# Kernel tuning notes

Hardware: AMD Instinct MI355X
Metric: run time of the kernel (lower is better)

The kernel has to match this reference:

```python
import jax, jax.numpy as jnp
import numpy as np

B, N, K, E, H, A = 16384, 200000, 16, 256, 2, 64
HD = E // H  # head_dim = 128


def setup_inputs() -> dict:
    key = jax.random.key(0)
    ks = jax.random.split(key, 10)
    s = 0.02
    return {
        "center_idx": jax.random.randint(ks[0], (B,), 0, N),
        "emb_table": jax.random.normal(ks[1], (N, E), jnp.float32),
        "neighbor_idx": jax.random.randint(ks[2], (N, K), 0, N),
        "neighbor_wt": jax.random.uniform(ks[3], (N, K), dtype=jnp.float32),
        # per-head attention MLP: Linear(2E -> A), GELU, Linear(A -> 1); stacked over heads
        "attn_W1": jax.random.normal(ks[4], (H, 2 * E, A), jnp.float32) * s,
        "attn_b1": jnp.zeros((H, A), jnp.float32),
        "attn_W2": jax.random.normal(ks[5], (H, A), jnp.float32) * s,
        "attn_b2": jnp.zeros((H,), jnp.float32),
        # per-head gate: Linear(HD -> HD), torch convention y = x @ W.T + b
        "gate_W": jax.random.normal(ks[6], (H, HD, HD), jnp.float32) * s,
        "gate_b": jnp.zeros((H, HD), jnp.float32),
        "out_W": jax.random.normal(ks[7], (E, E), jnp.float32) * s,
        "out_b": jnp.zeros((E,), jnp.float32),
    }


def reference(center_idx, emb_table, neighbor_idx, neighbor_wt,
              attn_W1, attn_b1, attn_W2, attn_b2,
              gate_W, gate_b, out_W, out_b):
    valid = center_idx >= 0                                      # [B]
    safe = jnp.maximum(center_idx, 0)
    center = jnp.where(valid[:, None], emb_table[safe], 0.0)      # [B,E]

    nb_idx = neighbor_idx[safe]                                   # [B,K]
    nb_wt = neighbor_wt[safe]                                     # [B,K]
    nb_mask = nb_idx >= 0
    nb_emb = emb_table[jnp.maximum(nb_idx, 0)]                    # [B,K,E]

    pair = jnp.concatenate(
        [jnp.broadcast_to(center[:, None, :], nb_emb.shape), nb_emb], axis=-1)  # [B,K,2E]

    # both attention heads in one einsum (exact GELU, as torch nn.GELU default)
    h1 = jax.nn.gelu(jnp.einsum('bkf,hfa->bkha', pair, attn_W1) + attn_b1,
                     approximate=False)                           # [B,K,H,A]
    logits = jnp.einsum('bkha,ha->bhk', h1, attn_W2) + attn_b2[None, :, None]  # [B,H,K]
    logits = logits + jnp.log(nb_wt + 1e-8)[:, None, :]
    logits = jnp.where(nb_mask[:, None, :], logits, -jnp.inf)
    has_any = jnp.any(nb_mask, axis=-1)                           # [B]
    logits = jnpp_where = jnp.where(has_any[:, None, None], logits, 0.0)
    w = jax.nn.softmax(logits, axis=-1)                           # [B,H,K]; dropout is identity in eval

    # aggregated[:, h*HD:(h+1)*HD] for head h == head-block of head-h weighted sum
    nb_r = nb_emb.reshape(-1, K, H, HD)
    agg = jnp.einsum('bhk,bkhd->bhd', w, nb_r)                    # [B,H,HD]

    c_head = center.reshape(-1, H, HD)
    gate = jax.nn.sigmoid(jnp.einsum('bhd,hed->bhe', c_head, gate_W) + gate_b)
    combined = (c_head + gate * agg).reshape(-1, E)               # [B,E]

    out = combined @ out_W.T + out_b
    return jnp.where(valid[:, None], out, center)
```

## Files before the change

### kernel.cpp

```cpp
#include <hip/hip_runtime.h>
#include <hip/hip_bf16.h>
#include <math.h>

#define BATCH   16384
#define NTAB    200000
#define KNB     16
#define EDIM    256
#define HEADS   2
#define ADIM    64
#define HD      128

typedef __attribute__((ext_vector_type(8))) short  short8;
typedef __attribute__((ext_vector_type(4))) float  f32x4;
typedef __attribute__((ext_vector_type(8))) unsigned short ushort8;
typedef __attribute__((ext_vector_type(4))) unsigned short ushort4v;

__device__ __forceinline__ unsigned short f2b(float f) {
    union { float f; unsigned u; } x; x.f = f;
    unsigned r = x.u + 0x7fffu + ((x.u >> 16) & 1u);
    return (unsigned short)(r >> 16);
}
__device__ __forceinline__ float b2f(unsigned short h) {
    union { unsigned u; float f; } x; x.u = ((unsigned)h) << 16;
    return x.f;
}

static const size_t OFF_TBL  = 0;
static const size_t OFF_T    = OFF_TBL  + (size_t)NTAB * 256 * 2;
static const size_t OFF_CG   = OFF_T    + (size_t)NTAB * 128 * 2;
static const size_t OFF_COMB = OFF_CG   + (size_t)BATCH * 384 * 2;
static const size_t OFF_WCAT = OFF_COMB + (size_t)BATCH * 256 * 2;
static const size_t OFF_W1B  = OFF_WCAT + 384 * 256 * 2;
static const size_t OFF_OUTW = OFF_W1B  + 128 * 256 * 2;
static const size_t OFF_BCAT = OFF_OUTW + 256 * 256 * 2;

__global__ __launch_bounds__(256) void repack_kernel(
    const float* __restrict__ W1, const float* __restrict__ gateW,
    const float* __restrict__ outW,
    const float* __restrict__ b1, const float* __restrict__ gateB,
    unsigned short* __restrict__ WcatT, unsigned short* __restrict__ W1bT,
    unsigned short* __restrict__ outWT, float* __restrict__ bcat)
{
    int i = blockIdx.x * 256 + threadIdx.x;
    {
        int c = i >> 8, f = i & 255;
        float v;
        if (c < 128) {
            int h = c >> 6, a = c & 63;
            v = W1[h * 32768 + f * 64 + a];
        } else {
            int e = c - 128;
            int h = e >> 7;
            v = ((e >> 7) == (f >> 7)) ? gateW[h * 16384 + (e & 127) * 128 + (f & 127)] : 0.f;
        }
        WcatT[i] = f2b(v);
    }
    if (i < 32768) {
        int c = i >> 8, f = i & 255;
        int h = c >> 6, a = c & 63;
        W1bT[i] = f2b(W1[h * 32768 + (256 + f) * 64 + a]);
    }
    if (i < 65536) outWT[i] = f2b(outW[i]);
    if (i < 384) bcat[i] = (i < 128) ? b1[i] : gateB[i - 128];
}

template<int AMODE, bool OUT_BF16, bool HAS_BIAS, bool HAS_MASK, bool WRITE_ABF>
__global__ __launch_bounds__(256) void gemm_mfma(
    const float* __restrict__ Af, const unsigned short* __restrict__ Ab,
    unsigned short* __restrict__ AoutBf,
    const int* __restrict__ gather,
    const unsigned short* __restrict__ Wt, int Nw,
    const float* __restrict__ bias, const int* __restrict__ mask,
    void* __restrict__ Cout, int M)
{
    __shared__ unsigned short sA[128 * 32];
    __shared__ unsigned short sB[128 * 32];
    __shared__ int s_idx[128];

    const int t = threadIdx.x;
    const int row0    = blockIdx.x * 128;
    const int colBase = blockIdx.y * 128;

    if (AMODE == 1 && t < 128) s_idx[t] = gather[row0 + t];

    const int wv   = t >> 6;
    const int wr   = wv >> 1, wc = wv & 1;
    const int lane = t & 63;
    const int l15  = lane & 15;
    const int quad = lane >> 4;

    f32x4 acc[4][4];
#pragma unroll
    for (int a = 0; a < 4; ++a)
#pragma unroll
        for (int b = 0; b < 4; ++b) acc[a][b] = (f32x4)0.f;

    for (int k0 = 0; k0 < 256; k0 += 32) {
        __syncthreads();
        if (AMODE == 0) {
#pragma unroll
            for (int l = 0; l < 4; ++l) {
                int p = t + l * 256;
                int row = p >> 3, seg = p & 7;
                int gr = row0 + row;
                int sr = gr < M ? gr : M - 1;
                const float4 v = *(const float4*)&Af[(size_t)sr * 256 + k0 + seg * 4];
                ushort4v h;
                h.x = f2b(v.x); h.y = f2b(v.y); h.z = f2b(v.z); h.w = f2b(v.w);
                *(ushort4v*)&sA[row * 32 + seg * 4] = h;
                if (WRITE_ABF && gr < M)
                    *(ushort4v*)&AoutBf[(size_t)gr * 256 + k0 + seg * 4] = h;
            }
        } else {
#pragma unroll
            for (int l = 0; l < 2; ++l) {
                int p = t + l * 256;
                int row = p >> 2, seg = p & 3;
                int sr;
                if (AMODE == 1) { int g = s_idx[row]; sr = g < 0 ? 0 : g; }
                else            { sr = row0 + row; if (sr > M - 1) sr = M - 1; }
                const unsigned short* gsrc = Ab + (size_t)sr * 256 + k0 + seg * 8;
                unsigned short* lbase = sA + (size_t)(p & ~63) * 8;
                __builtin_amdgcn_global_load_lds(
                    (const __attribute__((address_space(1))) void*)gsrc,
                    (__attribute__((address_space(3))) void*)lbase, 16, 0, 0);
            }
        }
#pragma unroll
        for (int l = 0; l < 2; ++l) {
            int p = t + l * 256;
            int n = p >> 2, seg = p & 3;
            const unsigned short* gsrc = Wt + (size_t)(colBase + n) * 256 + k0 + seg * 8;
            unsigned short* lbase = sB + (size_t)(p & ~63) * 8;
            __builtin_amdgcn_global_load_lds(
                (const __attribute__((address_space(1))) void*)gsrc,
                (__attribute__((address_space(3))) void*)lbase, 16, 0, 0);
        }
        __syncthreads();

        short8 af[4], bfr[4];
#pragma unroll
        for (int tr = 0; tr < 4; ++tr)
            af[tr] = *(const short8*)&sA[(wr * 64 + tr * 16 + l15) * 32 + quad * 8];
#pragma unroll
        for (int tc = 0; tc < 4; ++tc)
            bfr[tc] = *(const short8*)&sB[(wc * 64 + tc * 16 + l15) * 32 + quad * 8];
#pragma unroll
        for (int tr = 0; tr < 4; ++tr)
#pragma unroll
            for (int tc = 0; tc < 4; ++tc)
                acc[tr][tc] = __builtin_amdgcn_mfma_f32_16x16x32_bf16(
                    af[tr], bfr[tc], acc[tr][tc], 0, 0, 0);
    }

    float bcol[4];
#pragma unroll
    for (int tc = 0; tc < 4; ++tc)
        bcol[tc] = HAS_BIAS ? bias[colBase + wc * 64 + tc * 16 + l15] : 0.f;

#pragma unroll
    for (int tr = 0; tr < 4; ++tr) {
#pragma unroll
        for (int r = 0; r < 4; ++r) {
            int rowg = row0 + wr * 64 + tr * 16 + quad * 4 + r;
            if (rowg < M) {
                bool zero = HAS_MASK && (mask[rowg] < 0);
#pragma unroll
                for (int tc = 0; tc < 4; ++tc) {
                    int col = colBase + wc * 64 + tc * 16 + l15;
                    float v = zero ? 0.f : acc[tr][tc][r] + bcol[tc];
                    if (OUT_BF16)
                        ((unsigned short*)Cout)[(size_t)rowg * Nw + col] = f2b(v);
                    else
                        ((float*)Cout)[(size_t)rowg * Nw + col] = v;
                }
            }
        }
    }
}

__global__ __launch_bounds__(256) void epilogue_kernel(
    const unsigned short* __restrict__ tableBf, const int* __restrict__ center_idx,
    const int* __restrict__ nb_idx_tab, const float* __restrict__ nb_wt_tab,
    const unsigned short* __restrict__ T, const unsigned short* __restrict__ cg,
    const float* __restrict__ W2, const float* __restrict__ b2,
    unsigned short* __restrict__ comb)
{
    const int b = blockIdx.x;
    const int t = threadIdx.x;

    __shared__ float s_cg[384];
    __shared__ float s_w2[128];
    __shared__ float s_logit[32];
    __shared__ float s_wmx[32];
    __shared__ int   s_nb[16];
    __shared__ float s_wt[16];

    const int ci   = center_idx[b];
    const int safe = ci < 0 ? 0 : ci;

    if (t < 16) {
        s_nb[t] = nb_idx_tab[(size_t)safe * KNB + t];
        s_wt[t] = nb_wt_tab[(size_t)safe * KNB + t];
    }
    if (t < 128) s_w2[t] = W2[t];
    for (int i = t; i < 384; i += 256) s_cg[i] = b2f(cg[(size_t)b * 384 + i]);
    const float ctr = (ci < 0) ? 0.f : b2f(tableBf[(size_t)ci * 256 + t]);
    __syncthreads();

    {
        const int k = t >> 4, s = t & 15;
        const int nb = s_nb[k];
        const int ns = nb < 0 ? 0 : nb;
        const ushort8 tv = *(const ushort8*)&T[(size_t)ns * 128 + s * 8];
        float partial = 0.f;
#pragma unroll
        for (int j = 0; j < 8; ++j) {
            int c = s * 8 + j;
            float v = b2f(tv[j]) + s_cg[c];
            float g = 0.5f * v * (1.f + erff(v * 0.70710678118654752440f));
            partial = fmaf(g, s_w2[c], partial);
        }
        partial += __shfl_xor(partial, 1, 64);
        partial += __shfl_xor(partial, 2, 64);
        partial += __shfl_xor(partial, 4, 64);
        if (s == 0) s_logit[k] = partial;
        if (s == 8) s_logit[16 + k] = partial;
    }
    __syncthreads();

    if (t < 32) {
        const int h = t >> 4, k = t & 15;
        const int nb = s_nb[k];
        unsigned long long bm = __ballot(nb >= 0);
        const bool hasany = ((bm >> (h * 16)) & 0xFFFFull) != 0ull;
        float L = (nb >= 0)
            ? s_logit[h * 16 + k] + b2[h] + logf(s_wt[k] + 1e-8f)
            : -INFINITY;
        float m = L;
        m = fmaxf(m, __shfl_xor(m, 1, 16));
        m = fmaxf(m, __shfl_xor(m, 2, 16));
        m = fmaxf(m, __shfl_xor(m, 4, 16));
        m = fmaxf(m, __shfl_xor(m, 8, 16));
        float e = (nb >= 0) ? expf(L - m) : 0.f;
        float ssum = e;
        ssum += __shfl_xor(ssum, 1, 16);
        ssum += __shfl_xor(ssum, 2, 16);
        ssum += __shfl_xor(ssum, 4, 16);
        ssum += __shfl_xor(ssum, 8, 16);
        s_wmx[t] = hasany ? e / ssum : (1.f / 16.f);
    }
    __syncthreads();

    const int h = t >> 7;
    float agg = 0.f;
#pragma unroll
    for (int k = 0; k < 16; ++k) {
        int nb = s_nb[k];
        int ns = nb < 0 ? 0 : nb;
        agg = fmaf(s_wmx[h * 16 + k], b2f(tableBf[(size_t)ns * 256 + t]), agg);
    }
    float gl   = s_cg[128 + t];
    float gate = 1.f / (1.f + expf(-gl));
    comb[(size_t)b * 256 + t] = f2b(ctr + gate * agg);
}

extern "C" void kernel_launch(void* const* d_in, const int* in_sizes, int n_in,
                              void* d_out, int out_size, void* d_ws, size_t ws_size,
                              hipStream_t stream)
{
    const int*   center_idx = (const int*)  d_in[0];
    const float* emb_table  = (const float*)d_in[1];
    const int*   nb_idx     = (const int*)  d_in[2];
    const float* nb_wt      = (const float*)d_in[3];
    const float* attn_W1    = (const float*)d_in[4];
    const float* attn_b1    = (const float*)d_in[5];
    const float* attn_W2    = (const float*)d_in[6];
    const float* attn_b2    = (const float*)d_in[7];
    const float* gate_W     = (const float*)d_in[8];
    const float* gate_b     = (const float*)d_in[9];
    const float* out_W      = (const float*)d_in[10];
    const float* out_b      = (const float*)d_in[11];
    float* out = (float*)d_out;

    char* ws = (char*)d_ws;
    unsigned short* tableBf = (unsigned short*)(ws + OFF_TBL);
    unsigned short* T       = (unsigned short*)(ws + OFF_T);
    unsigned short* cgB     = (unsigned short*)(ws + OFF_CG);
    unsigned short* comb    = (unsigned short*)(ws + OFF_COMB);
    unsigned short* WcatT   = (unsigned short*)(ws + OFF_WCAT);
    unsigned short* W1bT    = (unsigned short*)(ws + OFF_W1B);
    unsigned short* outWT   = (unsigned short*)(ws + OFF_OUTW);
    float*          bcat    = (float*)         (ws + OFF_BCAT);

    repack_kernel<<<384, 256, 0, stream>>>(attn_W1, gate_W, out_W, attn_b1, gate_b,
                                           WcatT, W1bT, outWT, bcat);

    gemm_mfma<0, true, false, false, true><<<dim3((NTAB + 127) / 128, 1), 256, 0, stream>>>(
        emb_table, nullptr, tableBf, nullptr, W1bT, 128, nullptr, nullptr, T, NTAB);

    gemm_mfma<1, true, true, false, false><<<dim3(BATCH / 128, 3), 256, 0, stream>>>(
        nullptr, tableBf, nullptr, center_idx, WcatT, 384, bcat, nullptr, cgB, BATCH);

    epilogue_kernel<<<BATCH, 256, 0, stream>>>(
        tableBf, center_idx, nb_idx, nb_wt, T, cgB, attn_W2, attn_b2, comb);

    gemm_mfma<2, false, true, true, false><<<dim3(BATCH / 128, 2), 256, 0, stream>>>(
        nullptr, comb, nullptr, nullptr, outWT, 256, out_b, center_idx, out, BATCH);
}
```

Baseline: 461.8 us.

## Replace table-wide GEMM with register-resident weight streaming kernel

Measured after the change: 468.5 us. About the same (+1.4%).

```diff
diff --git a/kernel.cpp b/kernel.cpp
--- a/kernel.cpp
+++ b/kernel.cpp
@@ -64,10 +64,62 @@
     if (i < 384) bcat[i] = (i < 128) ? b1[i] : gateB[i - 128];
 }
 
-template<int AMODE, bool OUT_BF16, bool HAS_BIAS, bool HAS_MASK, bool WRITE_ABF>
+__global__ __launch_bounds__(256) void tgemm_stream(
+    const float* __restrict__ Af, const unsigned short* __restrict__ Wt,
+    unsigned short* __restrict__ T, unsigned short* __restrict__ tableBf)
+{
+    const int t    = threadIdx.x;
+    const int wv   = t >> 6;
+    const int lane = t & 63;
+    const int l15  = lane & 15;
+    const int quad = lane >> 4;
+
+    short8 bfrag[2][8];
+#pragma unroll
+    for (int tc = 0; tc < 2; ++tc)
+#pragma unroll
+        for (int kk = 0; kk < 8; ++kk)
+            bfrag[tc][kk] = *(const short8*)&Wt[(size_t)(wv * 32 + tc * 16 + l15) * 256 + kk * 32 + quad * 8];
+
+    for (int rt = blockIdx.x; rt < NTAB / 16; rt += gridDim.x) {
+        const int row0 = rt * 16;
+        const float* arow = Af + (size_t)(row0 + l15) * 256 + quad * 8;
+
+        float4 a32[16];
+#pragma unroll
+        for (int kk = 0; kk < 8; ++kk) {
+            a32[kk * 2]     = *(const float4*)(arow + kk * 32);
+            a32[kk * 2 + 1] = *(const float4*)(arow + kk * 32 + 4);
+        }
+
+        f32x4 acc0 = (f32x4)0.f, acc1 = (f32x4)0.f;
+#pragma unroll
+        for (int kk = 0; kk < 8; ++kk) {
+            const float* pa = (const float*)&a32[kk * 2];
+            ushort8 u;
+#pragma unroll
+            for (int j = 0; j < 8; ++j) u[j] = f2b(pa[j]);
+            short8 af;
+#pragma unroll
+            for (int j = 0; j < 8; ++j) af[j] = (short)u[j];
+            acc0 = __builtin_amdgcn_mfma_f32_16x16x32_bf16(af, bfrag[0][kk], acc0, 0, 0, 0);
+            acc1 = __builtin_amdgcn_mfma_f32_16x16x32_bf16(af, bfrag[1][kk], acc1, 0, 0, 0);
+            if ((kk >> 1) == wv)
+                *(ushort8*)&tableBf[(size_t)(row0 + l15) * 256 + kk * 32 + quad * 8] = u;
+        }
+
+#pragma unroll
+        for (int r = 0; r < 4; ++r) {
+            int row = row0 + quad * 4 + r;
+            T[(size_t)row * 128 + wv * 32 + l15]      = f2b(acc0[r]);
+            T[(size_t)row * 128 + wv * 32 + 16 + l15] = f2b(acc1[r]);
+        }
+    }
+}
+
+template<int AMODE, bool OUT_BF16, bool HAS_BIAS, bool HAS_MASK>
 __global__ __launch_bounds__(256) void gemm_mfma(
-    const float* __restrict__ Af, const unsigned short* __restrict__ Ab,
-    unsigned short* __restrict__ AoutBf,
+    const unsigned short* __restrict__ Ab,
     const int* __restrict__ gather,
     const unsigned short* __restrict__ Wt, int Nw,
     const float* __restrict__ bias, const int* __restrict__ mask,
@@ -97,34 +149,18 @@
 
     for (int k0 = 0; k0 < 256; k0 += 32) {
         __syncthreads();
-        if (AMODE == 0) {
-#pragma unroll
-            for (int l = 0; l < 4; ++l) {
-                int p = t + l * 256;
-                int row = p >> 3, seg = p & 7;
-                int gr = row0 + row;
-                int sr = gr < M ? gr : M - 1;
-                const float4 v = *(const float4*)&Af[(size_t)sr * 256 + k0 + seg * 4];
-                ushort4v h;
-                h.x = f2b(v.x); h.y = f2b(v.y); h.z = f2b(v.z); h.w = f2b(v.w);
-                *(ushort4v*)&sA[row * 32 + seg * 4] = h;
-                if (WRITE_ABF && gr < M)
-                    *(ushort4v*)&AoutBf[(size_t)gr * 256 + k0 + seg * 4] = h;
-            }
-        } else {
-#pragma unroll
-            for (int l = 0; l < 2; ++l) {
-                int p = t + l * 256;
-                int row = p >> 2, seg = p & 3;
-                int sr;
-                if (AMODE == 1) { int g = s_idx[row]; sr = g < 0 ? 0 : g; }
-                else            { sr = row0 + row; if (sr > M - 1) sr = M - 1; }
-                const unsigned short* gsrc = Ab + (size_t)sr * 256 + k0 + seg * 8;
-                unsigned short* lbase = sA + (size_t)(p & ~63) * 8;
-                __builtin_amdgcn_global_load_lds(
-                    (const __attribute__((address_space(1))) void*)gsrc,
-                    (__attribute__((address_space(3))) void*)lbase, 16, 0, 0);
-            }
+#pragma unroll
+        for (int l = 0; l < 2; ++l) {
+            int p = t + l * 256;
+            int row = p >> 2, seg = p & 3;
+            int sr;
+            if (AMODE == 1) { int g = s_idx[row]; sr = g < 0 ? 0 : g; }
+            else            { sr = row0 + row; if (sr > M - 1) sr = M - 1; }
+            const unsigned short* gsrc = Ab + (size_t)sr * 256 + k0 + seg * 8;
+            unsigned short* lbase = sA + (size_t)(p & ~63) * 8;
+            __builtin_amdgcn_global_load_lds(
+                (const __attribute__((address_space(1))) void*)gsrc,
+                (__attribute__((address_space(3))) void*)lbase, 16, 0, 0);
         }
 #pragma unroll
         for (int l = 0; l < 2; ++l) {
@@ -296,15 +332,14 @@
     repack_kernel<<<384, 256, 0, stream>>>(attn_W1, gate_W, out_W, attn_b1, gate_b,
                                            WcatT, W1bT, outWT, bcat);
 
-    gemm_mfma<0, true, false, false, true><<<dim3((NTAB + 127) / 128, 1), 256, 0, stream>>>(
-        emb_table, nullptr, tableBf, nullptr, W1bT, 128, nullptr, nullptr, T, NTAB);
-
-    gemm_mfma<1, true, true, false, false><<<dim3(BATCH / 128, 3), 256, 0, stream>>>(
-        nullptr, tableBf, nullptr, center_idx, WcatT, 384, bcat, nullptr, cgB, BATCH);
+    tgemm_stream<<<2048, 256, 0, stream>>>(emb_table, W1bT, T, tableBf);
+
+    gemm_mfma<1, true, true, false><<<dim3(BATCH / 128, 3), 256, 0, stream>>>(
+        tableBf, center_idx, WcatT, 384, bcat, nullptr, cgB, BATCH);
 
     epilogue_kernel<<<BATCH, 256, 0, stream>>>(
         tableBf, center_idx, nb_idx, nb_wt, T, cgB, attn_W2, attn_b2, comb);
 
-    gemm_mfma<2, false, true, true, false><<<dim3(BATCH / 128, 2), 256, 0, stream>>>(
-        nullptr, comb, nullptr, nullptr, outWT, 256, out_b, center_idx, out, BATCH);
-}
+    gemm_mfma<2, false, true, true><<<dim3(BATCH / 128, 2), 256, 0, stream>>>(
+        comb, nullptr, outWT, 256, out_b, center_idx, out, BATCH);
+}
```
